# Kernel optimization log

Measured on AMD Instinct MI355X. Metric: run time of the kernel, lower is better.

The kernel has to match this reference:

```python
import jax, jax.numpy as jnp
import numpy as np

B, N, E = 4, 4096, 2048
H_DIM = 2048
HEADS = 16
DH = H_DIM // HEADS
LN_EPS = 1e-5


def setup_inputs() -> dict:
    key = jax.random.key(0)
    ks = jax.random.split(key, 10)
    s = 1.0 / np.sqrt(E)
    so = 1.0 / np.sqrt(H_DIM)
    return {
        "x": jax.random.normal(ks[0], (B, N, E), jnp.float32),
        "Wqk": jax.random.normal(ks[1], (E, H_DIM), jnp.float32) * s,
        "bqk": jnp.zeros((H_DIM,), jnp.float32),
        "Wv": jax.random.normal(ks[2], (E, H_DIM), jnp.float32) * s,
        "bv": jnp.zeros((H_DIM,), jnp.float32),
        "Wu": jax.random.normal(ks[3], (E, H_DIM), jnp.float32) * s,
        "bu": jnp.zeros((H_DIM,), jnp.float32),
        "Wo": jax.random.normal(ks[4], (H_DIM, E), jnp.float32) * so,
        "bo": jnp.zeros((E,), jnp.float32),
        "ln_g": jnp.ones((H_DIM,), jnp.float32),
        "ln_b": jnp.zeros((H_DIM,), jnp.float32),
    }


def _heads(t):
    # [b, n, (h d)] -> [b, h, n, d]
    b, n, _ = t.shape
    return t.reshape(b, n, HEADS, DH).transpose(0, 2, 1, 3)


def _layernorm(x, g, b):
    mu = jnp.mean(x, axis=-1, keepdims=True)
    var = jnp.mean(jnp.square(x - mu), axis=-1, keepdims=True)
    return (x - mu) * jax.lax.rsqrt(var + LN_EPS) * g + b


def reference(x, Wqk, bqk, Wv, bv, Wu, bu, Wo, bo, ln_g, ln_b):
    # y = x (self-attention); qk_proj shared for q and k
    q = x @ Wqk + bqk
    k = x @ Wqk + bqk
    v = jax.nn.silu(x @ Wv + bv)   # uv_act = swish
    u = jax.nn.silu(x @ Wu + bu)
    q = jax.nn.elu(_heads(q))      # act = elu (applied after head split)
    kh = jax.nn.elu(_heads(k))
    vh = _heads(v)
    # non-causal associative form: kv = k^T v, out = q @ kv
    kv = jnp.einsum('bhnd,bhne->bhde', kh, vh)
    out = jnp.einsum('bhnd,bhde->bhne', q, kv)
    out = out.transpose(0, 2, 1, 3).reshape(x.shape[0], x.shape[1], H_DIM)
    out = _layernorm(out, ln_g, ln_b)
    out = u * out
    return out @ Wo + bo
```

## Files before the change

### kernel.cpp

```cpp
#include <hip/hip_runtime.h>

typedef __attribute__((ext_vector_type(8))) short short8;
typedef __attribute__((ext_vector_type(4))) float floatx4;

__device__ __forceinline__ float b2f(unsigned short u) {
  union { unsigned int i; float f; } c; c.i = ((unsigned int)u) << 16; return c.f;
}
__device__ __forceinline__ unsigned short f2b(float f) {
  union { float f; unsigned int i; } c; c.f = f;
  unsigned int i = c.i;
  return (unsigned short)((i + 0x7FFFu + ((i >> 16) & 1u)) >> 16);
}
__device__ __forceinline__ float elu_f(float x) {
  return x > 0.f ? x : (expf(x) - 1.f);
}
__device__ __forceinline__ float silu_f(float x) {
  return x / (1.f + expf(-x));
}
__device__ __forceinline__ void async16(const unsigned short* g, unsigned short* l) {
  __builtin_amdgcn_global_load_lds(
      (const __attribute__((address_space(1))) void*)g,
      (__attribute__((address_space(3))) void*)l, 16, 0, 0);
}
__device__ __forceinline__ floatx4 mfma16(short8 a, short8 b, floatx4 c) {
  return __builtin_amdgcn_mfma_f32_16x16x32_bf16(a, b, c, 0, 0, 0);
}

__global__ __launch_bounds__(256) void detect_dtype(
    const unsigned int* __restrict__ x, int* __restrict__ cnt) {
  int t = threadIdx.x;
  int c = 0;
  for (int i = t; i < 4096; i += 256) {
    unsigned int lo = x[i] & 0xFFFFu;
    unsigned int e = (lo >> 7) & 0xFFu;
    if (e >= 0x70u && e <= 0x8Fu) c++;
  }
#pragma unroll
  for (int off = 32; off > 0; off >>= 1) c += __shfl_down(c, off, 64);
  if ((t & 63) == 0) atomicAdd(cnt, c);
}
__device__ __forceinline__ bool is_f32(const int* flag) { return flag[0] < 2048; }

__global__ __launch_bounds__(256) void convert_x(
    const void* __restrict__ x, unsigned short* __restrict__ xb,
    const int* __restrict__ flag) {
  if (!is_f32(flag)) return;
  size_t i = ((size_t)blockIdx.x * 256 + threadIdx.x) * 8;
  const float* xf = (const float*)x;
  float4 a = *(const float4*)(xf + i);
  float4 b = *(const float4*)(xf + i + 4);
  unsigned short p[8] = {f2b(a.x), f2b(a.y), f2b(a.z), f2b(a.w),
                         f2b(b.x), f2b(b.y), f2b(b.z), f2b(b.w)};
  *(uint4*)(xb + i) = *(uint4*)p;
}

__global__ __launch_bounds__(256) void transpose2048(
    const void* __restrict__ src, unsigned short* __restrict__ dst,
    const int* __restrict__ flag) {
  const bool f32 = is_f32(flag);
  __shared__ unsigned short tile[32][33];
  int bx = blockIdx.x * 32;
  int by = blockIdx.y * 32;
  int tx = threadIdx.x & 31;
  int ty = threadIdx.x >> 5;
  for (int i = ty; i < 32; i += 8) {
    size_t idx = (size_t)(by + i) * 2048 + bx + tx;
    tile[i][tx] = f32 ? f2b(((const float*)src)[idx]) : ((const unsigned short*)src)[idx];
  }
  __syncthreads();
  for (int i = ty; i < 32; i += 8)
    dst[(size_t)(bx + i) * 2048 + by + tx] = tile[tx][i];
}

__global__ __launch_bounds__(512, 2) void gemm256(
    const unsigned short* __restrict__ A0,
    const unsigned short* __restrict__ A1, int a_sel,
    const unsigned short* __restrict__ WT,
    const void* __restrict__ bias,
    void* __restrict__ C, int c_ext,
    int K, int Nc, int act, const int* __restrict__ flag) {
  const bool f32 = is_f32(flag);
  const unsigned short* A = (a_sel && f32) ? A1 : A0;
  __shared__ __align__(16) unsigned short lds[8 * 8192];
#define CH(b, m, ks) (lds + ((((b)*2 + (m)) * 2 + (ks)) * 8192))
  const int nbx = gridDim.x;
  const int flat = blockIdx.y * nbx + blockIdx.x;
  const int nwg = nbx * gridDim.y;
  const int cpx = nwg >> 3;
  const int nf = (flat & 7) * cpx + (flat >> 3);
  const int bn = (nf % nbx) * 256;
  const int bm = (nf / nbx) * 256;
  const int t = threadIdx.x;
  const int lane = t & 63;
  const int wave = t >> 6;
  const int lm = lane & 15;
  const int quad = lane >> 4;
  const int wm = (wave >> 2) * 128;
  const int wn = (wave & 3) * 64;
  const int srow = lane >> 2;
  const int scol = (((lane & 3) ^ ((lane >> 3) & 3)) * 8);
  const int rq = (quad ^ ((lm >> 1) & 3)) * 8;
  const int NT = K >> 6;

  floatx4 acc[8][4] = {};

  auto stageA = [&](int kt, int ks, unsigned short* ch) {
#pragma unroll
    for (int c = 0; c < 2; ++c) {
      int rr = c * 128 + wave * 16;
      async16(A + (size_t)(bm + rr + srow) * K + kt + ks * 32 + scol, ch + rr * 32);
    }
  };
  auto stageB = [&](int kt, int ks, unsigned short* ch) {
#pragma unroll
    for (int c = 0; c < 2; ++c) {
      int rr = c * 128 + wave * 16;
      async16(WT + (size_t)(bn + rr + srow) * K + kt + ks * 32 + scol, ch + rr * 32);
    }
  };

  stageA(0, 0, CH(0, 0, 0));
  stageB(0, 0, CH(0, 1, 0));
  stageA(0, 1, CH(0, 0, 1));
  stageB(0, 1, CH(0, 1, 1));
  asm volatile("s_waitcnt vmcnt(4)" ::: "memory");
  asm volatile("s_barrier" ::: "memory");

  for (int ti = 0; ti < NT; ++ti) {
    const int buf = ti & 1, nb = buf ^ 1;
    const int ktn = (ti + 1 < NT ? ti + 1 : ti) << 6;
    const unsigned short* cA0 = CH(buf, 0, 0);
    const unsigned short* cB0 = CH(buf, 1, 0);
    const unsigned short* cA1 = CH(buf, 0, 1);
    const unsigned short* cB1 = CH(buf, 1, 1);
    short8 af[8], bf0, bf1;

#pragma unroll
    for (int mi = 0; mi < 8; ++mi)
      af[mi] = *(const short8*)(cA0 + (wm + mi * 16 + lm) * 32 + rq);
    bf0 = *(const short8*)(cB0 + (wn + lm) * 32 + rq);
    bf1 = *(const short8*)(cB0 + (wn + 16 + lm) * 32 + rq);
    stageA(ktn, 0, CH(nb, 0, 0));
    asm volatile("s_barrier" ::: "memory");
    asm volatile("s_waitcnt lgkmcnt(0)" ::: "memory");
    __builtin_amdgcn_sched_barrier(0);
    __builtin_amdgcn_s_setprio(1);
#pragma unroll
    for (int mi = 0; mi < 8; ++mi) {
      acc[mi][0] = mfma16(af[mi], bf0, acc[mi][0]);
      acc[mi][1] = mfma16(af[mi], bf1, acc[mi][1]);
    }
    __builtin_amdgcn_s_setprio(0);
    asm volatile("s_barrier" ::: "memory");

    bf0 = *(const short8*)(cB0 + (wn + 32 + lm) * 32 + rq);
    bf1 = *(const short8*)(cB0 + (wn + 48 + lm) * 32 + rq);
    stageB(ktn, 0, CH(nb, 1, 0));
    asm volatile("s_barrier" ::: "memory");
    asm volatile("s_waitcnt lgkmcnt(0)" ::: "memory");
    __builtin_amdgcn_sched_barrier(0);
    __builtin_amdgcn_s_setprio(1);
#pragma unroll
    for (int mi = 0; mi < 8; ++mi) {
      acc[mi][2] = mfma16(af[mi], bf0, acc[mi][2]);
      acc[mi][3] = mfma16(af[mi], bf1, acc[mi][3]);
    }
    __builtin_amdgcn_s_setprio(0);
    asm volatile("s_waitcnt vmcnt(4)" ::: "memory");
    asm volatile("s_barrier" ::: "memory");

#pragma unroll
    for (int mi = 0; mi < 8; ++mi)
      af[mi] = *(const short8*)(cA1 + (wm + mi * 16 + lm) * 32 + rq);
    bf0 = *(const short8*)(cB1 + (wn + lm) * 32 + rq);
    bf1 = *(const short8*)(cB1 + (wn + 16 + lm) * 32 + rq);
    stageA(ktn, 1, CH(nb, 0, 1));
    asm volatile("s_barrier" ::: "memory");
    asm volatile("s_waitcnt lgkmcnt(0)" ::: "memory");
    __builtin_amdgcn_sched_barrier(0);
    __builtin_amdgcn_s_setprio(1);
#pragma unroll
    for (int mi = 0; mi < 8; ++mi) {
      acc[mi][0] = mfma16(af[mi], bf0, acc[mi][0]);
      acc[mi][1] = mfma16(af[mi], bf1, acc[mi][1]);
    }
    __builtin_amdgcn_s_setprio(0);
    asm volatile("s_barrier" ::: "memory");

    bf0 = *(const short8*)(cB1 + (wn + 32 + lm) * 32 + rq);
    bf1 = *(const short8*)(cB1 + (wn + 48 + lm) * 32 + rq);
    stageB(ktn, 1, CH(nb, 1, 1));
    asm volatile("s_barrier" ::: "memory");
    asm volatile("s_waitcnt lgkmcnt(0)" ::: "memory");
    __builtin_amdgcn_sched_barrier(0);
    __builtin_amdgcn_s_setprio(1);
#pragma unroll
    for (int mi = 0; mi < 8; ++mi) {
      acc[mi][2] = mfma16(af[mi], bf0, acc[mi][2]);
      acc[mi][3] = mfma16(af[mi], bf1, acc[mi][3]);
    }
    __builtin_amdgcn_s_setprio(0);
    asm volatile("s_waitcnt vmcnt(4)" ::: "memory");
    asm volatile("s_barrier" ::: "memory");
  }
  asm volatile("s_waitcnt vmcnt(0)" ::: "memory");

#pragma unroll
  for (int ni = 0; ni < 4; ++ni) {
    int col = bn + wn + ni * 16 + lm;
    float bv = f32 ? ((const float*)bias)[col] : b2f(((const unsigned short*)bias)[col]);
#pragma unroll
    for (int mi = 0; mi < 8; ++mi) {
#pragma unroll
      for (int r = 0; r < 4; ++r) {
        int row = bm + wm + mi * 16 + quad * 4 + r;
        float v = acc[mi][ni][r] + bv;
        if (act == 1) v = silu_f(v);
        size_t idx = (size_t)row * Nc + col;
        if (c_ext && f32) ((float*)C)[idx] = v;
        else ((unsigned short*)C)[idx] = f2b(v);
      }
    }
  }
#undef CH
}

__global__ __launch_bounds__(256) void kv_accum(
    const unsigned short* __restrict__ QK,
    const unsigned short* __restrict__ V,
    float* __restrict__ kvT, int chunk) {
  const int bh = blockIdx.x;
  const int sp = blockIdx.y;
  const int b = bh >> 4, h = bh & 15;
  __shared__ __align__(16) unsigned short Kt[128][72];
  __shared__ __align__(16) unsigned short Vt[128][72];
  const int t = threadIdx.x;
  const int lane = t & 63, wave = t >> 6;
  const int lm = lane & 15, quad = lane >> 4;
  const int wm = (wave >> 1) * 64, wn = (wave & 1) * 64;
  floatx4 acc[4][4] = {};
  const size_t base = (size_t)b * 4096 * 2048 + (size_t)h * 128;
  const int nl = t & 63;
  const int dg0 = t >> 6;
  for (int n0 = sp * chunk; n0 < (sp + 1) * chunk; n0 += 64) {
#pragma unroll
    for (int i = 0; i < 4; ++i) {
      int dg = dg0 + 4 * i;
      union { uint4 u; unsigned short s[8]; } vk, vv;
      vk.u = *(const uint4*)(QK + base + (size_t)(n0 + nl) * 2048 + dg * 8);
      vv.u = *(const uint4*)(V + base + (size_t)(n0 + nl) * 2048 + dg * 8);
#pragma unroll
      for (int j = 0; j < 8; ++j) {
        Kt[dg * 8 + j][nl] = f2b(elu_f(b2f(vk.s[j])));
        Vt[dg * 8 + j][nl] = vv.s[j];
      }
    }
    __syncthreads();
#pragma unroll
    for (int ks = 0; ks < 2; ++ks) {
      short8 af[4], bf[4];
#pragma unroll
      for (int mi = 0; mi < 4; ++mi)
        af[mi] = *(const short8*)&Kt[wm + mi * 16 + lm][ks * 32 + quad * 8];
#pragma unroll
      for (int ni = 0; ni < 4; ++ni)
        bf[ni] = *(const short8*)&Vt[wn + ni * 16 + lm][ks * 32 + quad * 8];
#pragma unroll
      for (int mi = 0; mi < 4; ++mi)
#pragma unroll
        for (int ni = 0; ni < 4; ++ni)
          acc[mi][ni] = __builtin_amdgcn_mfma_f32_16x16x32_bf16(
              af[mi], bf[ni], acc[mi][ni], 0, 0, 0);
    }
    __syncthreads();
  }
  float* dst = kvT + (size_t)bh * 128 * 128;
#pragma unroll
  for (int mi = 0; mi < 4; ++mi)
#pragma unroll
    for (int ni = 0; ni < 4; ++ni)
#pragma unroll
      for (int r = 0; r < 4; ++r) {
        int d = wm + mi * 16 + quad * 4 + r;
        int e = wn + ni * 16 + lm;
        atomicAdd(&dst[e * 128 + d], acc[mi][ni][r]);
      }
}

__global__ __launch_bounds__(256) void attn_out(
    const unsigned short* __restrict__ QK,
    const float* __restrict__ kvT,
    unsigned short* __restrict__ O) {
  const int flat0 = blockIdx.y * 16 + blockIdx.x;
  const int nf = (flat0 & 7) * 256 + (flat0 >> 3);
  const int h = nf & 15;
  const int bm = (nf >> 4) * 128;
  const int b = bm >> 12;
  const int bh = b * 16 + h;
  __shared__ __align__(16) unsigned short As[128][136];
  __shared__ __align__(16) unsigned short Bs[128][136];
  const int t = threadIdx.x;
  const int lane = t & 63, wave = t >> 6;
  const int lm = lane & 15, quad = lane >> 4;
  const int wm = (wave >> 1) * 64, wn = (wave & 1) * 64;
  {
    const int r0 = t >> 4;
    const int g = t & 15;
#pragma unroll
    for (int i = 0; i < 8; ++i) {
      int r = r0 + 16 * i;
      union { uint4 u; unsigned short s[8]; } vq, w;
      vq.u = *(const uint4*)(QK + (size_t)(bm + r) * 2048 + h * 128 + g * 8);
#pragma unroll
      for (int j = 0; j < 8; ++j) w.s[j] = f2b(elu_f(b2f(vq.s[j])));
      *(uint4*)&As[r][g * 8] = w.u;
    }
    const int e0 = t >> 5;
    const int gg = t & 31;
    const float* kvp = kvT + (size_t)bh * 16384;
#pragma unroll
    for (int i = 0; i < 16; ++i) {
      int e = e0 + 8 * i;
      float4 f = *(const float4*)(kvp + e * 128 + gg * 4);
      unsigned short o4[4] = {f2b(f.x), f2b(f.y), f2b(f.z), f2b(f.w)};
      *(uint2*)&Bs[e][gg * 4] = *(uint2*)o4;
    }
  }
  __syncthreads();
  floatx4 acc[4][4] = {};
#pragma unroll
  for (int ks = 0; ks < 4; ++ks) {
    short8 af[4], bf[4];
#pragma unroll
    for (int mi = 0; mi < 4; ++mi)
      af[mi] = *(const short8*)&As[wm + mi * 16 + lm][ks * 32 + quad * 8];
#pragma unroll
    for (int ni = 0; ni < 4; ++ni)
      bf[ni] = *(const short8*)&Bs[wn + ni * 16 + lm][ks * 32 + quad * 8];
#pragma unroll
    for (int mi = 0; mi < 4; ++mi)
#pragma unroll
      for (int ni = 0; ni < 4; ++ni)
        acc[mi][ni] = __builtin_amdgcn_mfma_f32_16x16x32_bf16(
            af[mi], bf[ni], acc[mi][ni], 0, 0, 0);
  }
#pragma unroll
  for (int mi = 0; mi < 4; ++mi)
#pragma unroll
    for (int ni = 0; ni < 4; ++ni)
#pragma unroll
      for (int r = 0; r < 4; ++r) {
        int row = bm + wm + mi * 16 + quad * 4 + r;
        int e = wn + ni * 16 + lm;
        O[(size_t)row * 2048 + h * 128 + e] = f2b(acc[mi][ni][r]);
      }
}

__global__ __launch_bounds__(256) void ln_mul(
    const unsigned short* __restrict__ O,
    const unsigned short* __restrict__ U,
    const void* __restrict__ g,
    const void* __restrict__ bb,
    unsigned short* __restrict__ T, const int* __restrict__ flag) {
  const bool f32 = is_f32(flag);
  const int row = blockIdx.x;
  const int t = threadIdx.x;
  const unsigned short* o = O + (size_t)row * 2048;
  float vals[8];
  float s = 0.f, s2 = 0.f;
#pragma unroll
  for (int i = 0; i < 8; ++i) {
    float f = b2f(o[t + 256 * i]);
    vals[i] = f;
    s += f;
    s2 += f * f;
  }
#pragma unroll
  for (int off = 32; off > 0; off >>= 1) {
    s += __shfl_down(s, off, 64);
    s2 += __shfl_down(s2, off, 64);
  }
  __shared__ float ps[4], ps2[4];
  int lane = t & 63, wave = t >> 6;
  if (lane == 0) { ps[wave] = s; ps2[wave] = s2; }
  __syncthreads();
  float S = ps[0] + ps[1] + ps[2] + ps[3];
  float S2 = ps2[0] + ps2[1] + ps2[2] + ps2[3];
  float mu = S * (1.f / 2048.f);
  float var = S2 * (1.f / 2048.f) - mu * mu;
  float rs = rsqrtf(var + 1e-5f);
#pragma unroll
  for (int i = 0; i < 8; ++i) {
    int c = t + 256 * i;
    float gv = f32 ? ((const float*)g)[c] : b2f(((const unsigned short*)g)[c]);
    float bv = f32 ? ((const float*)bb)[c] : b2f(((const unsigned short*)bb)[c]);
    float nv = (vals[i] - mu) * rs * gv + bv;
    float uu = b2f(U[(size_t)row * 2048 + c]);
    T[(size_t)row * 2048 + c] = f2b(nv * uu);
  }
}

extern "C" void kernel_launch(void* const* d_in, const int* in_sizes, int n_in,
                              void* d_out, int out_size, void* d_ws, size_t ws_size,
                              hipStream_t stream) {
  const void* x   = d_in[0];
  const void* Wqk = d_in[1];
  const void* bqk = d_in[2];
  const void* Wv  = d_in[3];
  const void* bv  = d_in[4];
  const void* Wu  = d_in[5];
  const void* bu  = d_in[6];
  const void* Wo  = d_in[7];
  const void* bo  = d_in[8];
  const void* lng = d_in[9];
  const void* lnb = d_in[10];

  char* ws = (char*)d_ws;
  const size_t MB = 1024 * 1024;
  int* flag = (int*)ws;
  unsigned short* WT   = (unsigned short*)(ws + 1 * MB);
  unsigned short* buf0 = (unsigned short*)(ws + 16 * MB);
  unsigned short* buf1 = (unsigned short*)(ws + 80 * MB);
  float* kvT = (float*)(ws + 144 * MB);
  unsigned short* xb = (unsigned short*)(ws + 148 * MB);

  dim3 tb(256);
  dim3 gb(512);
  dim3 ggrid(8, 64);
  hipMemsetAsync(flag, 0, 4096, stream);
  hipMemsetAsync(kvT, 0, (size_t)64 * 128 * 128 * 4, stream);
  detect_dtype<<<1, tb, 0, stream>>>((const unsigned int*)x, flag);
  convert_x<<<16384, tb, 0, stream>>>(x, xb, flag);

  const unsigned short* xs = (const unsigned short*)x;
  transpose2048<<<dim3(64, 64), tb, 0, stream>>>(Wqk, WT, flag);
  gemm256<<<ggrid, gb, 0, stream>>>(xs, xb, 1, WT, bqk, buf0, 0, 2048, 2048, 0, flag);
  transpose2048<<<dim3(64, 64), tb, 0, stream>>>(Wv, WT, flag);
  gemm256<<<ggrid, gb, 0, stream>>>(xs, xb, 1, WT, bv, buf1, 0, 2048, 2048, 1, flag);
  kv_accum<<<dim3(64, 8), tb, 0, stream>>>(buf0, buf1, kvT, 512);
  attn_out<<<dim3(16, 128), tb, 0, stream>>>(buf0, kvT, buf1);
  transpose2048<<<dim3(64, 64), tb, 0, stream>>>(Wu, WT, flag);
  gemm256<<<ggrid, gb, 0, stream>>>(xs, xb, 1, WT, bu, buf0, 0, 2048, 2048, 1, flag);
  ln_mul<<<16384, tb, 0, stream>>>(buf1, buf0, lng, lnb, buf1, flag);
  transpose2048<<<dim3(64, 64), tb, 0, stream>>>(Wo, WT, flag);
  gemm256<<<ggrid, gb, 0, stream>>>(buf1, buf1, 0, WT, bo, d_out, 1, 2048, 2048, 0, flag);
}
```

Before: 1.084 ms.

## Simplify GEMM pipeline, stage bf16 epilogue through LDS, vectorize LayerNorm

The GEMM main loop drops the fine-grained interleaved staging with barriers and setprio. It now issues all next-tile async loads up front, runs both k-substeps of MFMAs, and waits on vmcnt(0) once per tile. The bf16 output epilogue writes results into a swizzled LDS tile, then stores coalesced 16-byte rows to global memory instead of scattered 2-byte stores. ln_mul switches to 8 contiguous elements per thread with uint4/float4 loads and stores. The simpler loop may lose load/compute overlap because each tile now waits fully on its loads.

```diff
diff --git a/kernel.cpp b/kernel.cpp
--- a/kernel.cpp
+++ b/kernel.cpp
@@ -123,103 +123,84 @@
   stageB(0, 0, CH(0, 1, 0));
   stageA(0, 1, CH(0, 0, 1));
   stageB(0, 1, CH(0, 1, 1));
-  asm volatile("s_waitcnt vmcnt(4)" ::: "memory");
+  asm volatile("s_waitcnt vmcnt(0)" ::: "memory");
   asm volatile("s_barrier" ::: "memory");
 
   for (int ti = 0; ti < NT; ++ti) {
     const int buf = ti & 1, nb = buf ^ 1;
     const int ktn = (ti + 1 < NT ? ti + 1 : ti) << 6;
-    const unsigned short* cA0 = CH(buf, 0, 0);
-    const unsigned short* cB0 = CH(buf, 1, 0);
-    const unsigned short* cA1 = CH(buf, 0, 1);
-    const unsigned short* cB1 = CH(buf, 1, 1);
-    short8 af[8], bf0, bf1;
-
-#pragma unroll
-    for (int mi = 0; mi < 8; ++mi)
-      af[mi] = *(const short8*)(cA0 + (wm + mi * 16 + lm) * 32 + rq);
-    bf0 = *(const short8*)(cB0 + (wn + lm) * 32 + rq);
-    bf1 = *(const short8*)(cB0 + (wn + 16 + lm) * 32 + rq);
+
     stageA(ktn, 0, CH(nb, 0, 0));
+    stageB(ktn, 0, CH(nb, 1, 0));
+    stageA(ktn, 1, CH(nb, 0, 1));
+    stageB(ktn, 1, CH(nb, 1, 1));
+
+#pragma unroll
+    for (int ks = 0; ks < 2; ++ks) {
+      const unsigned short* cA = CH(buf, 0, ks);
+      const unsigned short* cB = CH(buf, 1, ks);
+      short8 af[8], bf[4];
+#pragma unroll
+      for (int mi = 0; mi < 8; ++mi)
+        af[mi] = *(const short8*)(cA + (wm + mi * 16 + lm) * 32 + rq);
+#pragma unroll
+      for (int ni = 0; ni < 4; ++ni)
+        bf[ni] = *(const short8*)(cB + (wn + ni * 16 + lm) * 32 + rq);
+#pragma unroll
+      for (int mi = 0; mi < 8; ++mi)
+#pragma unroll
+        for (int ni = 0; ni < 4; ++ni)
+          acc[mi][ni] = mfma16(af[mi], bf[ni], acc[mi][ni]);
+    }
+
+    asm volatile("s_waitcnt vmcnt(0)" ::: "memory");
     asm volatile("s_barrier" ::: "memory");
-    asm volatile("s_waitcnt lgkmcnt(0)" ::: "memory");
-    __builtin_amdgcn_sched_barrier(0);
-    __builtin_amdgcn_s_setprio(1);
-#pragma unroll
-    for (int mi = 0; mi < 8; ++mi) {
-      acc[mi][0] = mfma16(af[mi], bf0, acc[mi][0]);
-      acc[mi][1] = mfma16(af[mi], bf1, acc[mi][1]);
-    }
-    __builtin_amdgcn_s_setprio(0);
-    asm volatile("s_barrier" ::: "memory");
-
-    bf0 = *(const short8*)(cB0 + (wn + 32 + lm) * 32 + rq);
-    bf1 = *(const short8*)(cB0 + (wn + 48 + lm) * 32 + rq);
-    stageB(ktn, 0, CH(nb, 1, 0));
-    asm volatile("s_barrier" ::: "memory");
-    asm volatile("s_waitcnt lgkmcnt(0)" ::: "memory");
-    __builtin_amdgcn_sched_barrier(0);
-    __builtin_amdgcn_s_setprio(1);
-#pragma unroll
-    for (int mi = 0; mi < 8; ++mi) {
-      acc[mi][2] = mfma16(af[mi], bf0, acc[mi][2]);
-      acc[mi][3] = mfma16(af[mi], bf1, acc[mi][3]);
-    }
-    __builtin_amdgcn_s_setprio(0);
-    asm volatile("s_waitcnt vmcnt(4)" ::: "memory");
-    asm volatile("s_barrier" ::: "memory");
-
-#pragma unroll
-    for (int mi = 0; mi < 8; ++mi)
-      af[mi] = *(const short8*)(cA1 + (wm + mi * 16 + lm) * 32 + rq);
-    bf0 = *(const short8*)(cB1 + (wn + lm) * 32 + rq);
-    bf1 = *(const short8*)(cB1 + (wn + 16 + lm) * 32 + rq);
-    stageA(ktn, 1, CH(nb, 0, 1));
-    asm volatile("s_barrier" ::: "memory");
-    asm volatile("s_waitcnt lgkmcnt(0)" ::: "memory");
-    __builtin_amdgcn_sched_barrier(0);
-    __builtin_amdgcn_s_setprio(1);
-#pragma unroll
-    for (int mi = 0; mi < 8; ++mi) {
-      acc[mi][0] = mfma16(af[mi], bf0, acc[mi][0]);
-      acc[mi][1] = mfma16(af[mi], bf1, acc[mi][1]);
-    }
-    __builtin_amdgcn_s_setprio(0);
-    asm volatile("s_barrier" ::: "memory");
-
-    bf0 = *(const short8*)(cB1 + (wn + 32 + lm) * 32 + rq);
-    bf1 = *(const short8*)(cB1 + (wn + 48 + lm) * 32 + rq);
-    stageB(ktn, 1, CH(nb, 1, 1));
-    asm volatile("s_barrier" ::: "memory");
-    asm volatile("s_waitcnt lgkmcnt(0)" ::: "memory");
-    __builtin_amdgcn_sched_barrier(0);
-    __builtin_amdgcn_s_setprio(1);
-#pragma unroll
-    for (int mi = 0; mi < 8; ++mi) {
-      acc[mi][2] = mfma16(af[mi], bf0, acc[mi][2]);
-      acc[mi][3] = mfma16(af[mi], bf1, acc[mi][3]);
-    }
-    __builtin_amdgcn_s_setprio(0);
-    asm volatile("s_waitcnt vmcnt(4)" ::: "memory");
-    asm volatile("s_barrier" ::: "memory");
-  }
-  asm volatile("s_waitcnt vmcnt(0)" ::: "memory");
-
-#pragma unroll
-  for (int ni = 0; ni < 4; ++ni) {
-    int col = bn + wn + ni * 16 + lm;
-    float bv = f32 ? ((const float*)bias)[col] : b2f(((const unsigned short*)bias)[col]);
-#pragma unroll
-    for (int mi = 0; mi < 8; ++mi) {
-#pragma unroll
-      for (int r = 0; r < 4; ++r) {
-        int row = bm + wm + mi * 16 + quad * 4 + r;
-        float v = acc[mi][ni][r] + bv;
-        if (act == 1) v = silu_f(v);
-        size_t idx = (size_t)row * Nc + col;
-        if (c_ext && f32) ((float*)C)[idx] = v;
-        else ((unsigned short*)C)[idx] = f2b(v);
+  }
+
+  if (c_ext && f32) {
+#pragma unroll
+    for (int ni = 0; ni < 4; ++ni) {
+      int col = bn + wn + ni * 16 + lm;
+      float bv = ((const float*)bias)[col];
+#pragma unroll
+      for (int mi = 0; mi < 8; ++mi) {
+#pragma unroll
+        for (int r = 0; r < 4; ++r) {
+          int row = bm + wm + mi * 16 + quad * 4 + r;
+          float v = acc[mi][ni][r] + bv;
+          if (act == 1) v = silu_f(v);
+          ((float*)C)[(size_t)row * Nc + col] = v;
+        }
       }
+    }
+  } else {
+    unsigned short* ot = lds;
+#pragma unroll
+    for (int ni = 0; ni < 4; ++ni) {
+      int col = wn + ni * 16 + lm;
+      float bv = f32 ? ((const float*)bias)[bn + col]
+                     : b2f(((const unsigned short*)bias)[bn + col]);
+#pragma unroll
+      for (int mi = 0; mi < 8; ++mi) {
+        int rbase = wm + mi * 16 + quad * 4;
+#pragma unroll
+        for (int r = 0; r < 4; ++r) {
+          float v = acc[mi][ni][r] + bv;
+          if (act == 1) v = silu_f(v);
+          ot[(rbase + r) * 256 + (col ^ (quad << 4))] = f2b(v);
+        }
+      }
+    }
+    __syncthreads();
+    unsigned short* Cs = (unsigned short*)C;
+#pragma unroll
+    for (int i = 0; i < 16; ++i) {
+      int c = t + 512 * i;
+      int row = c >> 5;
+      int k = c & 31;
+      int phys = (k * 8) ^ (((row >> 2) & 3) << 4);
+      uint4 v = *(const uint4*)&ot[row * 256 + phys];
+      *(uint4*)(Cs + (size_t)(bm + row) * Nc + bn + k * 8) = v;
     }
   }
 #undef CH
@@ -365,13 +346,15 @@
   const bool f32 = is_f32(flag);
   const int row = blockIdx.x;
   const int t = threadIdx.x;
-  const unsigned short* o = O + (size_t)row * 2048;
+  const size_t base = (size_t)row * 2048 + t * 8;
+  union { uint4 u; unsigned short s[8]; } vo, vu;
+  vo.u = *(const uint4*)(O + base);
   float vals[8];
   float s = 0.f, s2 = 0.f;
 #pragma unroll
-  for (int i = 0; i < 8; ++i) {
-    float f = b2f(o[t + 256 * i]);
-    vals[i] = f;
+  for (int j = 0; j < 8; ++j) {
+    float f = b2f(vo.s[j]);
+    vals[j] = f;
     s += f;
     s2 += f * f;
   }
@@ -389,15 +372,31 @@
   float mu = S * (1.f / 2048.f);
   float var = S2 * (1.f / 2048.f) - mu * mu;
   float rs = rsqrtf(var + 1e-5f);
-#pragma unroll
-  for (int i = 0; i < 8; ++i) {
-    int c = t + 256 * i;
-    float gv = f32 ? ((const float*)g)[c] : b2f(((const unsigned short*)g)[c]);
-    float bv = f32 ? ((const float*)bb)[c] : b2f(((const unsigned short*)bb)[c]);
-    float nv = (vals[i] - mu) * rs * gv + bv;
-    float uu = b2f(U[(size_t)row * 2048 + c]);
-    T[(size_t)row * 2048 + c] = f2b(nv * uu);
-  }
+  vu.u = *(const uint4*)(U + base);
+  float gv[8], bv[8];
+  if (f32) {
+    float4 g0 = *(const float4*)((const float*)g + t * 8);
+    float4 g1 = *(const float4*)((const float*)g + t * 8 + 4);
+    float4 b0 = *(const float4*)((const float*)bb + t * 8);
+    float4 b1 = *(const float4*)((const float*)bb + t * 8 + 4);
+    gv[0] = g0.x; gv[1] = g0.y; gv[2] = g0.z; gv[3] = g0.w;
+    gv[4] = g1.x; gv[5] = g1.y; gv[6] = g1.z; gv[7] = g1.w;
+    bv[0] = b0.x; bv[1] = b0.y; bv[2] = b0.z; bv[3] = b0.w;
+    bv[4] = b1.x; bv[5] = b1.y; bv[6] = b1.z; bv[7] = b1.w;
+  } else {
+    union { uint4 u; unsigned short s[8]; } vg, vb;
+    vg.u = *(const uint4*)((const unsigned short*)g + t * 8);
+    vb.u = *(const uint4*)((const unsigned short*)bb + t * 8);
+#pragma unroll
+    for (int j = 0; j < 8; ++j) { gv[j] = b2f(vg.s[j]); bv[j] = b2f(vb.s[j]); }
+  }
+  unsigned short outp[8];
+#pragma unroll
+  for (int j = 0; j < 8; ++j) {
+    float nv = (vals[j] - mu) * rs * gv[j] + bv[j];
+    outp[j] = f2b(nv * b2f(vu.s[j]));
+  }
+  *(uint4*)(T + base) = *(uint4*)outp;
 }
 
 extern "C" void kernel_launch(void* const* d_in, const int* in_sizes, int n_in,
```

After: 1.072 ms. About the same (-1.0%).
